# Performance work log

Hardware: AMD Instinct MI355X
Metric: run time of the kernel (lower is better)

The kernel has to match this reference:

```python
import math
import jax, jax.numpy as jnp
import numpy as np

NUM_HEADS = 16
INPUT_DIM = 1024
VALUES_DIM = 1024
HEAD_DIM = INPUT_DIM // NUM_HEADS


def _pos_embeddings(length, dim):
    # TENER positional encoding for `length` positions centered at 0: [length, dim]
    half = dim // 2
    position = jnp.arange(-(length // 2), length // 2, dtype=jnp.float32)[:, None]
    div_term = jnp.exp(jnp.arange(half, dtype=jnp.float32) * (-math.log(10000.0) / (half - 1)))
    ang = position * div_term[None, :]
    return jnp.concatenate([jnp.sin(ang), jnp.cos(ang)], axis=1)


def _shift(t):
    # [B,H,S,2S] -> [B,H,S,S] relative-position shift trick
    B, H, S, _ = t.shape
    t = jnp.concatenate([t, jnp.zeros((B, H, S, 1), t.dtype)], axis=-1)  # [B,H,S,2S+1]
    t = t.reshape(B, H, 2 * S + 1, S)[:, :, :-1].reshape(B, H, S, 2 * S)
    return t[..., S:]


def setup_inputs() -> dict:
    key = jax.random.key(0)
    ks = jax.random.split(key, 9)
    B, S, D, Dv = 2, 1024, INPUT_DIM, VALUES_DIM
    s = 1.0 / math.sqrt(D)
    return {
        "query": jax.random.normal(ks[0], (B, S, D), jnp.float32),
        "key": jax.random.normal(ks[1], (B, S, D), jnp.float32),
        "value": jax.random.normal(ks[2], (B, S, D), jnp.float32),
        "mask": jnp.ones((B, S), jnp.int32),
        "Wq": jax.random.normal(ks[3], (D, D), jnp.float32) * s,
        "bq": jnp.zeros((D,), jnp.float32),
        "Wv": jax.random.normal(ks[4], (Dv, D), jnp.float32) * s,
        "bv": jnp.zeros((Dv,), jnp.float32),
        "Wo": jax.random.normal(ks[5], (D, Dv), jnp.float32) * (1.0 / math.sqrt(Dv)),
        "bo": jnp.zeros((D,), jnp.float32),
        "v_bias": jax.random.normal(ks[6], (NUM_HEADS, HEAD_DIM), jnp.float32) * (1.0 / math.sqrt(HEAD_DIM)),
    }


def reference(query, key, value, mask, Wq, bq, Wv, bv, Wo, bo, v_bias):
    B, S, D = query.shape
    H, d = NUM_HEADS, HEAD_DIM
    dv = VALUES_DIM // H
    pos = _pos_embeddings(2 * S, d)  # [2S, d]

    k = key.reshape(B, S, H, d).transpose(0, 2, 1, 3)                       # [B,H,S,d] (no projection!)
    q = (query @ Wq.T + bq).reshape(B, S, H, d).transpose(0, 2, 1, 3)       # [B,H,S,d]
    v = (value @ Wv.T + bv).reshape(B, S, H, dv).transpose(0, 2, 1, 3)      # [B,H,S,dv]

    qk = jnp.einsum('bhqd,bhkd->bhqk', q, k)                                # [B,H,S,S]
    v_bias_rel = jnp.einsum('hd,ld->hl', v_bias, pos)[None, :, None, :]     # [1,H,1,2S]
    q_rel = jnp.einsum('bhqd,ld->bhql', q, pos)                             # [B,H,S,2S]
    rel = _shift(q_rel + v_bias_rel)                                        # [B,H,S,S]

    attn = jax.nn.softmax(qk + rel, axis=-1)                                # unscaled, unmasked (matches source)
    x = jnp.einsum('bhqk,bhkd->bhqd', attn, v)                              # [B,H,S,dv]
    x = x.transpose(0, 2, 1, 3).reshape(B, S, VALUES_DIM)
    return x @ Wo.T + bo
```

## Files before the change

### kernel.cpp

```cpp
#include <hip/hip_runtime.h>
#include <math.h>

#define SEQ 1024
#define DIM 1024
#define NH 16
#define HD 64
#define NB 2

typedef __attribute__((ext_vector_type(8))) short bf16x8;
typedef __attribute__((ext_vector_type(8))) _Float16 f16x8;
typedef __attribute__((ext_vector_type(4))) float f32x4;
typedef __attribute__((ext_vector_type(8))) unsigned short ushort8;
typedef __attribute__((ext_vector_type(4))) unsigned short ushort4v;

#define DT_CONST (-0.2971077539347156f)
#define FIXEDM 32.0f

__device__ __forceinline__ unsigned short f2bf(float x) {
    unsigned u = __float_as_uint(x);
    return (unsigned short)((u + 0x7fffu + ((u >> 16) & 1u)) >> 16);
}
__device__ __forceinline__ float bf2f(unsigned short h) {
    return __uint_as_float(((unsigned)h) << 16);
}
__device__ __forceinline__ unsigned short f2h(float x) {
    _Float16 h = (_Float16)x;
    return __builtin_bit_cast(unsigned short, h);
}

__device__ __forceinline__ void plain8(const float* __restrict__ s,
                                       unsigned short* __restrict__ h, int i) {
    float4 v0 = *(const float4*)&s[i];
    float4 v1 = *(const float4*)&s[i + 4];
    float vs[8] = {v0.x, v0.y, v0.z, v0.w, v1.x, v1.y, v1.z, v1.w};
    ushort8 hv;
    #pragma unroll
    for (int k = 0; k < 8; ++k) hv[k] = f2bf(vs[k]);
    *(ushort8*)&h[i] = hv;
}
__device__ __forceinline__ void plain8h(const float* __restrict__ s,
                                        unsigned short* __restrict__ h, int i) {
    float4 v0 = *(const float4*)&s[i];
    float4 v1 = *(const float4*)&s[i + 4];
    float vs[8] = {v0.x, v0.y, v0.z, v0.w, v1.x, v1.y, v1.z, v1.w};
    ushort8 hv;
    #pragma unroll
    for (int k = 0; k < 8; ++k) hv[k] = f2h(vs[k]);
    *(ushort8*)&h[i] = hv;
}

__global__ __launch_bounds__(256) void conv_all(
    const float* __restrict__ query, const float* __restrict__ key,
    const float* __restrict__ value, const float* __restrict__ Wq,
    const float* __restrict__ Wv, const float* __restrict__ Wo,
    unsigned short* __restrict__ Aqh,
    unsigned short* __restrict__ Khs,
    unsigned short* __restrict__ Vb,
    unsigned short* __restrict__ Wqh,
    unsigned short* __restrict__ Wvh,
    unsigned short* __restrict__ Woh,
    unsigned short* __restrict__ Kth)
{
    int i = (blockIdx.x * 256 + threadIdx.x) * 8;
    int r = blockIdx.y;
    const int NSMALL = DIM * DIM;
    if (r >= 3 && r <= 5 && i >= NSMALL) return;
    if (r == 6 && i >= SEQ * HD) return;
    switch (r) {
        case 0: plain8h(query, Aqh, i); break;
        case 1: plain8h(key,   Khs, i); break;
        case 2: plain8(value, Vb, i); break;
        case 3: plain8h(Wq, Wqh, i); break;
        case 4: plain8(Wv, Wvh, i); break;
        case 5: plain8(Wo, Woh, i); break;
        case 6: {
            ushort8 hv;
            #pragma unroll
            for (int k = 0; k < 8; ++k) {
                int idx = i + k;
                int j = idx >> 6;
                int c = idx & 63;
                int ii = c & 31;
                float dt = __expf((float)ii * DT_CONST);
                float ang = (float)j * dt;
                float val = (c < 32) ? sinf(ang) : cosf(ang);
                hv[k] = f2h(val);
            }
            *(ushort8*)&Kth[i] = hv;
            break;
        }
    }
}

#define QLD 72

__global__ __launch_bounds__(256) void qv_gemm(
    const unsigned short* __restrict__ Aqh, const unsigned short* __restrict__ Wqh,
    const float* __restrict__ bq,
    const unsigned short* __restrict__ Vb, const unsigned short* __restrict__ Wvh,
    const float* __restrict__ bv,
    const float* __restrict__ v_bias,
    unsigned short* __restrict__ Qh,
    unsigned short* __restrict__ vpT)
{
    __shared__ __align__(16) unsigned short smem[192 * QLD];
    unsigned short* sAh = smem;
    unsigned short* sWh = smem + 128 * QLD;

    const int K = DIM;
    bool isq = (blockIdx.z == 0);

    int tid = threadIdx.x;
    int lane = tid & 63;
    int w = tid >> 6;
    int l16 = lane & 15, quad = lane >> 4;
    int m0 = blockIdx.y * 128;
    int h = blockIdx.x;
    int n0 = h * 64;

    int ar = tid >> 2;
    int c0 = (tid & 3) << 3;
    int c1 = c0 + 32;

    const unsigned short* pAh0 = (isq ? Aqh : Vb) + (size_t)(m0 + ar) * K;
    const unsigned short* pAh1 = pAh0 + (size_t)64 * K;
    const unsigned short* pWh  = (isq ? Wqh : Wvh) + (size_t)(n0 + ar) * K;

    f32x4 acc[2][4];
    #pragma unroll
    for (int mq = 0; mq < 2; ++mq)
        #pragma unroll
        for (int nt = 0; nt < 4; ++nt)
            acc[mq][nt] = (f32x4){0.f, 0.f, 0.f, 0.f};

    ushort8 ra[4], rw[2];
    ra[0] = *(const ushort8*)(pAh0 + c0);  ra[1] = *(const ushort8*)(pAh0 + c1);
    ra[2] = *(const ushort8*)(pAh1 + c0);  ra[3] = *(const ushort8*)(pAh1 + c1);
    rw[0] = *(const ushort8*)(pWh + c0);   rw[1] = *(const ushort8*)(pWh + c1);

    for (int kk = 0; kk < K; kk += 64) {
        __syncthreads();
        *(ushort8*)&sAh[ar * QLD + c0] = ra[0];
        *(ushort8*)&sAh[ar * QLD + c1] = ra[1];
        *(ushort8*)&sAh[(ar + 64) * QLD + c0] = ra[2];
        *(ushort8*)&sAh[(ar + 64) * QLD + c1] = ra[3];
        *(ushort8*)&sWh[ar * QLD + c0] = rw[0];
        *(ushort8*)&sWh[ar * QLD + c1] = rw[1];
        if (kk + 64 < K) {
            int kn = kk + 64;
            ra[0] = *(const ushort8*)(pAh0 + kn + c0);  ra[1] = *(const ushort8*)(pAh0 + kn + c1);
            ra[2] = *(const ushort8*)(pAh1 + kn + c0);  ra[3] = *(const ushort8*)(pAh1 + kn + c1);
            rw[0] = *(const ushort8*)(pWh + kn + c0);   rw[1] = *(const ushort8*)(pWh + kn + c1);
        }
        __syncthreads();

        #pragma unroll
        for (int c = 0; c < 2; ++c) {
            int kpos = c * 32 + quad * 8;
            bf16x8 af[2];
            #pragma unroll
            for (int mq = 0; mq < 2; ++mq)
                af[mq] = *(const bf16x8*)&sAh[(w * 32 + mq * 16 + l16) * QLD + kpos];
            bf16x8 bhv[4];
            #pragma unroll
            for (int nt = 0; nt < 4; ++nt)
                bhv[nt] = *(const bf16x8*)&sWh[(nt * 16 + l16) * QLD + kpos];
            if (isq) {
                #pragma unroll
                for (int nt = 0; nt < 4; ++nt)
                    #pragma unroll
                    for (int mq = 0; mq < 2; ++mq)
                        acc[mq][nt] = __builtin_amdgcn_mfma_f32_16x16x32_f16(
                            __builtin_bit_cast(f16x8, af[mq]),
                            __builtin_bit_cast(f16x8, bhv[nt]), acc[mq][nt], 0, 0, 0);
            } else {
                #pragma unroll
                for (int nt = 0; nt < 4; ++nt)
                    #pragma unroll
                    for (int mq = 0; mq < 2; ++mq)
                        acc[mq][nt] = __builtin_amdgcn_mfma_f32_16x16x32_bf16(
                            af[mq], bhv[nt], acc[mq][nt], 0, 0, 0);
            }
        }
    }

    int b = m0 >> 10;

    if (isq) {
        float bql[4], vbs[2], vbc[2], dti[2];
        #pragma unroll
        for (int nt = 0; nt < 4; ++nt) bql[nt] = bq[h * 64 + nt * 16 + l16];
        #pragma unroll
        for (int t = 0; t < 2; ++t) {
            vbs[t] = v_bias[h * 64 + t * 16 + l16];
            vbc[t] = v_bias[h * 64 + 32 + t * 16 + l16];
            dti[t] = __expf((float)(t * 16 + l16) * DT_CONST);
        }
        #pragma unroll
        for (int mq = 0; mq < 2; ++mq) {
            #pragma unroll
            for (int reg = 0; reg < 4; ++reg) {
                int row = m0 + w * 32 + mq * 16 + quad * 4 + reg;
                int q = row & (SEQ - 1);
                size_t qbase = ((size_t)(b * NH + h) * SEQ + q) * 128;
                float hv[4];
                #pragma unroll
                for (int nt = 0; nt < 4; ++nt) hv[nt] = acc[mq][nt][reg] + bql[nt];
                #pragma unroll
                for (int nt = 0; nt < 4; ++nt)
                    Qh[qbase + nt * 16 + l16] = f2h(hv[nt]);
                #pragma unroll
                for (int t = 0; t < 2; ++t) {
                    float u = hv[t] + vbs[t];
                    float wv = hv[t + 2] + vbc[t];
                    float ang = (float)q * dti[t];
                    float C = cosf(ang), S = sinf(ang);
                    float cs = u * C + wv * S;
                    float cc = wv * C - u * S;
                    Qh[qbase + 64 + t * 16 + l16] = f2h(cs);
                    Qh[qbase + 96 + t * 16 + l16] = f2h(cc);
                }
            }
        }
    } else {
        __syncthreads();
        unsigned short* tb = smem;
        #pragma unroll
        for (int nt = 0; nt < 4; ++nt) {
            int d = nt * 16 + l16;
            float bcol = bv[n0 + d];
            #pragma unroll
            for (int mq = 0; mq < 2; ++mq)
                #pragma unroll
                for (int reg = 0; reg < 4; ++reg) {
                    int srow = w * 32 + mq * 16 + quad * 4 + reg;
                    tb[d * 136 + srow] = f2bf(acc[mq][nt][reg] + bcol);
                }
        }
        __syncthreads();
        int s0 = m0 & (SEQ - 1);
        #pragma unroll
        for (int i = tid; i < 1024; i += 256) {
            int dd = i >> 4;
            int j16 = i & 15;
            int sb = j16 >> 3;
            int posl = (j16 & 7) << 3;
            unsigned short tmp[8];
            #pragma unroll
            for (int k = 0; k < 8; ++k) {
                int pos = posl + k;
                int sl = (pos >> 2) + (pos & 3) * 16;
                tmp[k] = tb[dd * 136 + sb * 64 + sl];
            }
            *(ushort8*)&vpT[((size_t)((b * NH + h) * 64 + dd)) * SEQ + s0 + sb * 64 + posl] =
                *(ushort8*)tmp;
        }
    }
}

__global__ __launch_bounds__(256) void out_gemm(
    const unsigned short* __restrict__ Ab, const unsigned short* __restrict__ Woh,
    const float* __restrict__ bo, float* __restrict__ C)
{
    __shared__ unsigned short sA[64][32];
    __shared__ unsigned short sW[64][32];

    const int K = DIM, N = DIM;
    int tid = threadIdx.x;
    int lane = tid & 63;
    int w = tid >> 6;
    int l16 = lane & 15, quad = lane >> 4;
    int m0 = blockIdx.y * 64, n0 = blockIdx.x * 64;

    int ar = tid >> 2, ap = (tid & 3) << 3;

    const unsigned short* pA = Ab + (size_t)(m0 + ar) * K + ap;
    const unsigned short* pW = Woh + (size_t)(n0 + ar) * K + ap;

    f32x4 acc[4];
    #pragma unroll
    for (int nt = 0; nt < 4; ++nt) acc[nt] = (f32x4){0.f, 0.f, 0.f, 0.f};

    ushort8 a0 = *(const ushort8*)pA;
    ushort8 w0 = *(const ushort8*)pW;

    for (int kk = 0; kk < K; kk += 32) {
        __syncthreads();
        *(ushort8*)&sA[ar][ap] = a0;
        *(ushort8*)&sW[ar][ap] = w0;
        if (kk + 32 < K) {
            a0 = *(const ushort8*)(pA + kk + 32);
            w0 = *(const ushort8*)(pW + kk + 32);
        }
        __syncthreads();

        bf16x8 af = *(const bf16x8*)&sA[w * 16 + l16][quad * 8];
        bf16x8 bf[4];
        #pragma unroll
        for (int nt = 0; nt < 4; ++nt)
            bf[nt] = *(const bf16x8*)&sW[nt * 16 + l16][quad * 8];
        #pragma unroll
        for (int nt = 0; nt < 4; ++nt)
            acc[nt] = __builtin_amdgcn_mfma_f32_16x16x32_bf16(af, bf[nt], acc[nt], 0, 0, 0);
    }

    #pragma unroll
    for (int nt = 0; nt < 4; ++nt) {
        int col = n0 + nt * 16 + l16;
        float bcol = bo[col];
        #pragma unroll
        for (int reg = 0; reg < 4; ++reg) {
            int row = m0 + w * 16 + quad * 4 + reg;
            C[(size_t)row * N + col] = acc[nt][reg] + bcol;
        }
    }
}

#define LDK 136
#define LDV 72

__global__ __launch_bounds__(256) void attn_mfma(
    const unsigned short* __restrict__ Kh,
    const unsigned short* __restrict__ vpT,
    const unsigned short* __restrict__ Qh,
    const unsigned short* __restrict__ Kth,
    unsigned short* __restrict__ Opart,
    float* __restrict__ lsum)
{
    __shared__ unsigned short Ksh[64][LDK];
    __shared__ unsigned short Vt[64][LDV];
    __shared__ unsigned short Ps[128][LDV];

    int tid = threadIdx.x;
    int w = tid >> 6;
    int lane = tid & 63;
    int l16 = lane & 15;
    int quad = lane >> 4;

    int bid = blockIdx.x;
    int qt = bid & 7;
    int h = (bid >> 3) & 15;
    int b = (bid >> 7) & 1;
    int sp = bid >> 8;
    int q0 = qt << 7;
    int jb = sp << 3;

    int sr0 = tid >> 3, sp0 = (tid & 7) << 3;
    int sr1 = sr0 + 32;

    ushort8 pK0, pK1, pT0, pT1, pV0, pV1;
    {
        int j0 = jb << 6;
        size_t g0 = (size_t)(b * SEQ + j0 + sr0) * DIM + h * HD + sp0;
        size_t g1 = (size_t)(b * SEQ + j0 + sr1) * DIM + h * HD + sp0;
        pK0 = *(const ushort8*)&Kh[g0]; pK1 = *(const ushort8*)&Kh[g1];
        size_t t0 = (size_t)(j0 + sr0) * 64 + sp0, t1 = (size_t)(j0 + sr1) * 64 + sp0;
        pT0 = *(const ushort8*)&Kth[t0]; pT1 = *(const ushort8*)&Kth[t1];
        size_t v0 = ((size_t)((b * NH + h) * 64 + sr0)) * SEQ + j0 + sp0;
        size_t v1 = ((size_t)((b * NH + h) * 64 + sr1)) * SEQ + j0 + sp0;
        pV0 = *(const ushort8*)&vpT[v0]; pV1 = *(const ushort8*)&vpT[v1];
    }

    bf16x8 ah[2][4];
    #pragma unroll
    for (int half = 0; half < 2; ++half) {
        const unsigned short* gq = Qh + (((size_t)(b * NH + h)) * SEQ + q0 + half * 64) * 128;
        #pragma unroll
        for (int c = tid; c < 1024; c += 256) {
            int r = c >> 4, p = (c & 15) << 3;
            *(ushort8*)&Ksh[r][p] = *(const ushort8*)&gq[r * 128 + p];
        }
        __syncthreads();
        if ((w >> 1) == half) {
            #pragma unroll
            for (int mq = 0; mq < 2; ++mq)
                #pragma unroll
                for (int c = 0; c < 4; ++c)
                    ah[mq][c] = *(const bf16x8*)&Ksh[(w & 1) * 32 + mq * 16 + l16][c * 32 + quad * 8];
        }
        __syncthreads();
    }

    f32x4 oacc[2][4];
    f32x4 lacc[2];
    #pragma unroll
    for (int mq = 0; mq < 2; ++mq) {
        #pragma unroll
        for (int nb = 0; nb < 4; ++nb) oacc[mq][nb] = (f32x4){0.f, 0.f, 0.f, 0.f};
        lacc[mq] = (f32x4){0.f, 0.f, 0.f, 0.f};
    }

    bf16x8 onesv;
    #pragma unroll
    for (int k = 0; k < 8; ++k) onesv[k] = (short)0x3F80;

    for (int jt = 0; jt < 8; ++jt) {
        __syncthreads();
        *(ushort8*)&Ksh[sr0][sp0] = pK0;       *(ushort8*)&Ksh[sr1][sp0] = pK1;
        *(ushort8*)&Ksh[sr0][64 + sp0] = pT0;  *(ushort8*)&Ksh[sr1][64 + sp0] = pT1;
        *(ushort8*)&Vt[sr0][sp0] = pV0;        *(ushort8*)&Vt[sr1][sp0] = pV1;
        if (jt < 7) {
            int j0n = (jb + jt + 1) << 6;
            size_t g0 = (size_t)(b * SEQ + j0n + sr0) * DIM + h * HD + sp0;
            size_t g1 = (size_t)(b * SEQ + j0n + sr1) * DIM + h * HD + sp0;
            pK0 = *(const ushort8*)&Kh[g0]; pK1 = *(const ushort8*)&Kh[g1];
            size_t t0 = (size_t)(j0n + sr0) * 64 + sp0, t1 = (size_t)(j0n + sr1) * 64 + sp0;
            pT0 = *(const ushort8*)&Kth[t0]; pT1 = *(const ushort8*)&Kth[t1];
            size_t v0 = ((size_t)((b * NH + h) * 64 + sr0)) * SEQ + j0n + sp0;
            size_t v1 = ((size_t)((b * NH + h) * 64 + sr1)) * SEQ + j0n + sp0;
            pV0 = *(const ushort8*)&vpT[v0]; pV1 = *(const ushort8*)&vpT[v1];
        }
        __syncthreads();

        f32x4 sacc[2][4];
        #pragma unroll
        for (int mq = 0; mq < 2; ++mq)
            #pragma unroll
            for (int nb = 0; nb < 4; ++nb) sacc[mq][nb] = (f32x4){0.f, 0.f, 0.f, 0.f};
        #pragma unroll
        for (int nb = 0; nb < 4; ++nb) {
            #pragma unroll
            for (int c = 0; c < 4; ++c) {
                bf16x8 bh = *(const bf16x8*)&Ksh[nb * 16 + l16][c * 32 + quad * 8];
                #pragma unroll
                for (int mq = 0; mq < 2; ++mq)
                    sacc[mq][nb] = __builtin_amdgcn_mfma_f32_16x16x32_f16(
                        __builtin_bit_cast(f16x8, ah[mq][c]),
                        __builtin_bit_cast(f16x8, bh), sacc[mq][nb], 0, 0, 0);
            }
        }

        #pragma unroll
        for (int mq = 0; mq < 2; ++mq) {
            #pragma unroll
            for (int r = 0; r < 4; ++r) {
                float p0 = __expf(sacc[mq][0][r] - FIXEDM);
                float p1 = __expf(sacc[mq][1][r] - FIXEDM);
                float p2 = __expf(sacc[mq][2][r] - FIXEDM);
                float p3 = __expf(sacc[mq][3][r] - FIXEDM);
                int prow = w * 32 + mq * 16 + quad * 4 + r;
                ushort4v pv4;
                pv4.x = f2bf(p0); pv4.y = f2bf(p1); pv4.z = f2bf(p2); pv4.w = f2bf(p3);
                *(ushort4v*)&Ps[prow][l16 * 4] = pv4;
            }
        }
        __syncthreads();

        #pragma unroll
        for (int kc = 0; kc < 2; ++kc) {
            bf16x8 a[2];
            #pragma unroll
            for (int mq = 0; mq < 2; ++mq) {
                a[mq] = *(const bf16x8*)&Ps[w * 32 + mq * 16 + l16][kc * 32 + quad * 8];
                lacc[mq] = __builtin_amdgcn_mfma_f32_16x16x32_bf16(a[mq], onesv, lacc[mq], 0, 0, 0);
            }
            #pragma unroll
            for (int nb = 0; nb < 4; ++nb) {
                bf16x8 bv = *(const bf16x8*)&Vt[nb * 16 + l16][kc * 32 + quad * 8];
                #pragma unroll
                for (int mq = 0; mq < 2; ++mq)
                    oacc[mq][nb] = __builtin_amdgcn_mfma_f32_16x16x32_bf16(a[mq], bv, oacc[mq][nb], 0, 0, 0);
            }
        }
    }

    const size_t OOFF = (size_t)sp * NB * NH * SEQ * 64;
    const size_t LOFF = (size_t)sp * NB * NH * SEQ;
    #pragma unroll
    for (int mq = 0; mq < 2; ++mq) {
        #pragma unroll
        for (int r = 0; r < 4; ++r) {
            int qrow = q0 + w * 32 + mq * 16 + quad * 4 + r;
            size_t rowi = (size_t)(b * NH + h) * SEQ + qrow;
            #pragma unroll
            for (int nb = 0; nb < 4; ++nb)
                Opart[OOFF + rowi * 64 + nb * 16 + l16] = f2bf(oacc[mq][nb][r]);
            if (l16 == 0)
                lsum[LOFF + rowi] = lacc[mq][r];
        }
    }
}

__global__ __launch_bounds__(256) void attn_combine(
    const unsigned short* __restrict__ Opart, const float* __restrict__ lsum,
    unsigned short* __restrict__ xab)
{
    const size_t OOFF = (size_t)NB * NH * SEQ * 64;
    const size_t LOFF = (size_t)NB * NH * SEQ;
    int tid = threadIdx.x;
    int d = tid & 63;
    size_t r = (size_t)blockIdx.x * 4 + (tid >> 6);
    int q = (int)(r & (SEQ - 1));
    int h = (int)((r >> 10) & (NH - 1));
    int b = (int)(r >> 14);

    float inv = 1.f / (lsum[r] + lsum[LOFF + r]);
    float O0 = bf2f(Opart[r * 64 + d]);
    float O1 = bf2f(Opart[OOFF + r * 64 + d]);
    float o = (O0 + O1) * inv;
    xab[((size_t)(b * SEQ + q)) * DIM + h * HD + d] = f2bf(o);
}

extern "C" void kernel_launch(void* const* d_in, const int* in_sizes, int n_in,
                              void* d_out, int out_size, void* d_ws, size_t ws_size,
                              hipStream_t stream) {
    const float* query  = (const float*)d_in[0];
    const float* key    = (const float*)d_in[1];
    const float* value  = (const float*)d_in[2];
    const float* Wq     = (const float*)d_in[4];
    const float* bq     = (const float*)d_in[5];
    const float* Wv     = (const float*)d_in[6];
    const float* bv     = (const float*)d_in[7];
    const float* Wo     = (const float*)d_in[8];
    const float* bo     = (const float*)d_in[9];
    const float* v_bias = (const float*)d_in[10];

    float* out = (float*)d_out;
    char* base = (char*)d_ws;
    const size_t MB = 1024 * 1024;

    unsigned short* Aqh   = (unsigned short*)(base);
    unsigned short* vpT   = (unsigned short*)(base +  4 * MB);
    unsigned short* Khs   = (unsigned short*)(base +  8 * MB);
    unsigned short* Qh    = (unsigned short*)(base + 12 * MB);
    unsigned short* Wqh   = (unsigned short*)(base + 20 * MB);
    unsigned short* Vb    = (unsigned short*)(base + 22 * MB);
    unsigned short* Wvh   = (unsigned short*)(base + 26 * MB);
    unsigned short* Woh   = (unsigned short*)(base + 28 * MB);
    unsigned short* Kth   = (unsigned short*)(base + 30 * MB);
    unsigned short* xab   = (unsigned short*)(base + 31 * MB);
    float*          lsum  = (float*)(base + 35 * MB);
    unsigned short* Opart = (unsigned short*)(base + 36 * MB);

    const int M = NB * SEQ;

    dim3 cgrid(M * DIM / 2048, 7);
    conv_all<<<cgrid, 256, 0, stream>>>(query, key, value, Wq, Wv, Wo,
                                        Aqh, Khs, Vb, Wqh, Wvh, Woh, Kth);

    dim3 qvgrid(NH, M / 128, 2);
    qv_gemm<<<qvgrid, 256, 0, stream>>>(Aqh, Wqh, bq, Vb, Wvh, bv,
                                        v_bias, Qh, vpT);

    attn_mfma<<<2 * NB * NH * (SEQ / 128), 256, 0, stream>>>(Khs, vpT, Qh,
                                                             Kth, Opart, lsum);

    attn_combine<<<NB * NH * SEQ / 4, 256, 0, stream>>>(Opart, lsum, xab);

    dim3 ogrid(DIM / 64, M / 64);
    out_gemm<<<ogrid, 256, 0, stream>>>(xab, Woh, bo, out);
}
```

Measured before the change: 158.3 us.

## Remap block indices for L2 locality and widen out_gemm K-step to 64

Converts the qv_gemm, attn_mfma and out_gemm grids to 1D launches and remaps block IDs. The new order groups blocks that share input tiles, and on a multi-XCD GPU places related work on the same die for better L2 reuse. out_gemm now stages 64-wide K tiles with padded shared-memory rows, which halves the number of barrier pairs and avoids bank conflicts. This costs more shared memory and registers per block and depends on assumptions about how blocks are dispatched across dies.

```diff
diff --git a/kernel.cpp b/kernel.cpp
--- a/kernel.cpp
+++ b/kernel.cpp
@@ -108,15 +108,19 @@
     unsigned short* sWh = smem + 128 * QLD;
 
     const int K = DIM;
-    bool isq = (blockIdx.z == 0);
+
+    int bid = blockIdx.x;
+    int s = bid >> 3;
+    int y = (bid & 7) + 8 * (s & 1);
+    int h = (s >> 1) & 15;
+    bool isq = (s >> 5) == 0;
+    int m0 = y * 128;
+    int n0 = h * 64;
 
     int tid = threadIdx.x;
     int lane = tid & 63;
     int w = tid >> 6;
     int l16 = lane & 15, quad = lane >> 4;
-    int m0 = blockIdx.y * 128;
-    int h = blockIdx.x;
-    int n0 = h * 64;
 
     int ar = tid >> 2;
     int c0 = (tid & 3) << 3;
@@ -262,46 +266,58 @@
     const unsigned short* __restrict__ Ab, const unsigned short* __restrict__ Woh,
     const float* __restrict__ bo, float* __restrict__ C)
 {
-    __shared__ unsigned short sA[64][32];
-    __shared__ unsigned short sW[64][32];
+    __shared__ __align__(16) unsigned short sA[64 * QLD];
+    __shared__ __align__(16) unsigned short sW[64 * QLD];
 
     const int K = DIM, N = DIM;
+
+    int bid = blockIdx.x;
+    int n0 = ((bid >> 3) & 15) * 64;
+    int m0 = ((bid & 7) + 8 * (bid >> 7)) * 64;
+
     int tid = threadIdx.x;
     int lane = tid & 63;
     int w = tid >> 6;
     int l16 = lane & 15, quad = lane >> 4;
-    int m0 = blockIdx.y * 64, n0 = blockIdx.x * 64;
-
-    int ar = tid >> 2, ap = (tid & 3) << 3;
-
-    const unsigned short* pA = Ab + (size_t)(m0 + ar) * K + ap;
-    const unsigned short* pW = Woh + (size_t)(n0 + ar) * K + ap;
+
+    int ar = tid >> 2;
+    int c0 = (tid & 3) << 3;
+    int c1 = c0 + 32;
+
+    const unsigned short* pA = Ab + (size_t)(m0 + ar) * K;
+    const unsigned short* pW = Woh + (size_t)(n0 + ar) * K;
 
     f32x4 acc[4];
     #pragma unroll
     for (int nt = 0; nt < 4; ++nt) acc[nt] = (f32x4){0.f, 0.f, 0.f, 0.f};
 
-    ushort8 a0 = *(const ushort8*)pA;
-    ushort8 w0 = *(const ushort8*)pW;
-
-    for (int kk = 0; kk < K; kk += 32) {
-        __syncthreads();
-        *(ushort8*)&sA[ar][ap] = a0;
-        *(ushort8*)&sW[ar][ap] = w0;
-        if (kk + 32 < K) {
-            a0 = *(const ushort8*)(pA + kk + 32);
-            w0 = *(const ushort8*)(pW + kk + 32);
-        }
-        __syncthreads();
-
-        bf16x8 af = *(const bf16x8*)&sA[w * 16 + l16][quad * 8];
-        bf16x8 bf[4];
-        #pragma unroll
-        for (int nt = 0; nt < 4; ++nt)
-            bf[nt] = *(const bf16x8*)&sW[nt * 16 + l16][quad * 8];
-        #pragma unroll
-        for (int nt = 0; nt < 4; ++nt)
-            acc[nt] = __builtin_amdgcn_mfma_f32_16x16x32_bf16(af, bf[nt], acc[nt], 0, 0, 0);
+    ushort8 ra[2], rw[2];
+    ra[0] = *(const ushort8*)(pA + c0);  ra[1] = *(const ushort8*)(pA + c1);
+    rw[0] = *(const ushort8*)(pW + c0);  rw[1] = *(const ushort8*)(pW + c1);
+
+    for (int kk = 0; kk < K; kk += 64) {
+        __syncthreads();
+        *(ushort8*)&sA[ar * QLD + c0] = ra[0];
+        *(ushort8*)&sA[ar * QLD + c1] = ra[1];
+        *(ushort8*)&sW[ar * QLD + c0] = rw[0];
+        *(ushort8*)&sW[ar * QLD + c1] = rw[1];
+        if (kk + 64 < K) {
+            int kn = kk + 64;
+            ra[0] = *(const ushort8*)(pA + kn + c0);  ra[1] = *(const ushort8*)(pA + kn + c1);
+            rw[0] = *(const ushort8*)(pW + kn + c0);  rw[1] = *(const ushort8*)(pW + kn + c1);
+        }
+        __syncthreads();
+
+        #pragma unroll
+        for (int c = 0; c < 2; ++c) {
+            int kpos = c * 32 + quad * 8;
+            bf16x8 af = *(const bf16x8*)&sA[(w * 16 + l16) * QLD + kpos];
+            #pragma unroll
+            for (int nt = 0; nt < 4; ++nt) {
+                bf16x8 bh = *(const bf16x8*)&sW[(nt * 16 + l16) * QLD + kpos];
+                acc[nt] = __builtin_amdgcn_mfma_f32_16x16x32_bf16(af, bh, acc[nt], 0, 0, 0);
+            }
+        }
     }
 
     #pragma unroll
@@ -338,10 +354,11 @@
     int quad = lane >> 4;
 
     int bid = blockIdx.x;
-    int qt = bid & 7;
-    int h = (bid >> 3) & 15;
-    int b = (bid >> 7) & 1;
-    int sp = bid >> 8;
+    int g = bid & 63;
+    int qt = bid >> 6;
+    int h = g & 15;
+    int b = (g >> 4) & 1;
+    int sp = g >> 5;
     int q0 = qt << 7;
     int jb = sp << 3;
 
@@ -538,15 +555,12 @@
     conv_all<<<cgrid, 256, 0, stream>>>(query, key, value, Wq, Wv, Wo,
                                         Aqh, Khs, Vb, Wqh, Wvh, Woh, Kth);
 
-    dim3 qvgrid(NH, M / 128, 2);
-    qv_gemm<<<qvgrid, 256, 0, stream>>>(Aqh, Wqh, bq, Vb, Wvh, bv,
-                                        v_bias, Qh, vpT);
-
-    attn_mfma<<<2 * NB * NH * (SEQ / 128), 256, 0, stream>>>(Khs, vpT, Qh,
-                                                             Kth, Opart, lsum);
+    qv_gemm<<<512, 256, 0, stream>>>(Aqh, Wqh, bq, Vb, Wvh, bv,
+                                     v_bias, Qh, vpT);
+
+    attn_mfma<<<512, 256, 0, stream>>>(Khs, vpT, Qh, Kth, Opart, lsum);
 
     attn_combine<<<NB * NH * SEQ / 4, 256, 0, stream>>>(Opart, lsum, xab);
 
-    dim3 ogrid(DIM / 64, M / 64);
-    out_gemm<<<ogrid, 256, 0, stream>>>(xab, Woh, bo, out);
-}
+    out_gemm<<<512, 256, 0, stream>>>(xab, Woh, bo, out);
+}
```

Measured after the change: 157.4 us. About the same (-0.6%).

## Fuse input conversions into consumer GEMMs and fold split-combine into output GEMM

Applied to the files above, without the earlier changes.

Removes the standalone conversion pass that turned fp32 query/key/value/weights into half/bf16 copies. Each consumer kernel (qv_gemm, attn_mfma, the output GEMM) now loads fp32 directly and converts while writing to shared memory. The attention split-combine kernel is merged into the output projection, which normalizes the two partial outputs on the fly. This cuts several launches and the round-trip of intermediate buffers through memory. In exchange, global loads inside the GEMM loops are twice as wide and conversion ALU work is repeated across tiles that reread the same data.

```diff
diff --git a/kernel.cpp b/kernel.cpp
--- a/kernel.cpp
+++ b/kernel.cpp
@@ -27,77 +27,43 @@
     _Float16 h = (_Float16)x;
     return __builtin_bit_cast(unsigned short, h);
 }
-
-__device__ __forceinline__ void plain8(const float* __restrict__ s,
-                                       unsigned short* __restrict__ h, int i) {
-    float4 v0 = *(const float4*)&s[i];
-    float4 v1 = *(const float4*)&s[i + 4];
-    float vs[8] = {v0.x, v0.y, v0.z, v0.w, v1.x, v1.y, v1.z, v1.w};
-    ushort8 hv;
-    #pragma unroll
-    for (int k = 0; k < 8; ++k) hv[k] = f2bf(vs[k]);
-    *(ushort8*)&h[i] = hv;
-}
-__device__ __forceinline__ void plain8h(const float* __restrict__ s,
-                                        unsigned short* __restrict__ h, int i) {
-    float4 v0 = *(const float4*)&s[i];
-    float4 v1 = *(const float4*)&s[i + 4];
-    float vs[8] = {v0.x, v0.y, v0.z, v0.w, v1.x, v1.y, v1.z, v1.w};
-    ushort8 hv;
-    #pragma unroll
-    for (int k = 0; k < 8; ++k) hv[k] = f2h(vs[k]);
-    *(ushort8*)&h[i] = hv;
-}
-
-__global__ __launch_bounds__(256) void conv_all(
-    const float* __restrict__ query, const float* __restrict__ key,
-    const float* __restrict__ value, const float* __restrict__ Wq,
-    const float* __restrict__ Wv, const float* __restrict__ Wo,
-    unsigned short* __restrict__ Aqh,
-    unsigned short* __restrict__ Khs,
-    unsigned short* __restrict__ Vb,
-    unsigned short* __restrict__ Wqh,
-    unsigned short* __restrict__ Wvh,
-    unsigned short* __restrict__ Woh,
-    unsigned short* __restrict__ Kth)
+__device__ __forceinline__ ushort8 cvt8h(float4 a, float4 b) {
+    ushort8 r;
+    r[0] = f2h(a.x); r[1] = f2h(a.y); r[2] = f2h(a.z); r[3] = f2h(a.w);
+    r[4] = f2h(b.x); r[5] = f2h(b.y); r[6] = f2h(b.z); r[7] = f2h(b.w);
+    return r;
+}
+__device__ __forceinline__ ushort8 cvt8b(float4 a, float4 b) {
+    ushort8 r;
+    r[0] = f2bf(a.x); r[1] = f2bf(a.y); r[2] = f2bf(a.z); r[3] = f2bf(a.w);
+    r[4] = f2bf(b.x); r[5] = f2bf(b.y); r[6] = f2bf(b.z); r[7] = f2bf(b.w);
+    return r;
+}
+
+__global__ __launch_bounds__(256) void trig_gen(unsigned short* __restrict__ Kth)
 {
     int i = (blockIdx.x * 256 + threadIdx.x) * 8;
-    int r = blockIdx.y;
-    const int NSMALL = DIM * DIM;
-    if (r >= 3 && r <= 5 && i >= NSMALL) return;
-    if (r == 6 && i >= SEQ * HD) return;
-    switch (r) {
-        case 0: plain8h(query, Aqh, i); break;
-        case 1: plain8h(key,   Khs, i); break;
-        case 2: plain8(value, Vb, i); break;
-        case 3: plain8h(Wq, Wqh, i); break;
-        case 4: plain8(Wv, Wvh, i); break;
-        case 5: plain8(Wo, Woh, i); break;
-        case 6: {
-            ushort8 hv;
-            #pragma unroll
-            for (int k = 0; k < 8; ++k) {
-                int idx = i + k;
-                int j = idx >> 6;
-                int c = idx & 63;
-                int ii = c & 31;
-                float dt = __expf((float)ii * DT_CONST);
-                float ang = (float)j * dt;
-                float val = (c < 32) ? sinf(ang) : cosf(ang);
-                hv[k] = f2h(val);
-            }
-            *(ushort8*)&Kth[i] = hv;
-            break;
-        }
-    }
+    ushort8 hv;
+    #pragma unroll
+    for (int k = 0; k < 8; ++k) {
+        int idx = i + k;
+        int j = idx >> 6;
+        int c = idx & 63;
+        int ii = c & 31;
+        float dt = __expf((float)ii * DT_CONST);
+        float ang = (float)j * dt;
+        float val = (c < 32) ? sinf(ang) : cosf(ang);
+        hv[k] = f2h(val);
+    }
+    *(ushort8*)&Kth[i] = hv;
 }
 
 #define QLD 72
 
 __global__ __launch_bounds__(256) void qv_gemm(
-    const unsigned short* __restrict__ Aqh, const unsigned short* __restrict__ Wqh,
+    const float* __restrict__ query, const float* __restrict__ Wq,
     const float* __restrict__ bq,
-    const unsigned short* __restrict__ Vb, const unsigned short* __restrict__ Wvh,
+    const float* __restrict__ value, const float* __restrict__ Wv,
     const float* __restrict__ bv,
     const float* __restrict__ v_bias,
     unsigned short* __restrict__ Qh,
@@ -122,9 +88,9 @@
     int c0 = (tid & 3) << 3;
     int c1 = c0 + 32;
 
-    const unsigned short* pAh0 = (isq ? Aqh : Vb) + (size_t)(m0 + ar) * K;
-    const unsigned short* pAh1 = pAh0 + (size_t)64 * K;
-    const unsigned short* pWh  = (isq ? Wqh : Wvh) + (size_t)(n0 + ar) * K;
+    const float* pA0 = (isq ? query : value) + (size_t)(m0 + ar) * K;
+    const float* pA1 = pA0 + (size_t)64 * K;
+    const float* pW  = (isq ? Wq : Wv) + (size_t)(n0 + ar) * K;
 
     f32x4 acc[2][4];
     #pragma unroll
@@ -133,24 +99,39 @@
         for (int nt = 0; nt < 4; ++nt)
             acc[mq][nt] = (f32x4){0.f, 0.f, 0.f, 0.f};
 
-    ushort8 ra[4], rw[2];
-    ra[0] = *(const ushort8*)(pAh0 + c0);  ra[1] = *(const ushort8*)(pAh0 + c1);
-    ra[2] = *(const ushort8*)(pAh1 + c0);  ra[3] = *(const ushort8*)(pAh1 + c1);
-    rw[0] = *(const ushort8*)(pWh + c0);   rw[1] = *(const ushort8*)(pWh + c1);
+    float4 rf[6][2];
+    rf[0][0] = *(const float4*)(pA0 + c0); rf[0][1] = *(const float4*)(pA0 + c0 + 4);
+    rf[1][0] = *(const float4*)(pA0 + c1); rf[1][1] = *(const float4*)(pA0 + c1 + 4);
+    rf[2][0] = *(const float4*)(pA1 + c0); rf[2][1] = *(const float4*)(pA1 + c0 + 4);
+    rf[3][0] = *(const float4*)(pA1 + c1); rf[3][1] = *(const float4*)(pA1 + c1 + 4);
+    rf[4][0] = *(const float4*)(pW + c0);  rf[4][1] = *(const float4*)(pW + c0 + 4);
+    rf[5][0] = *(const float4*)(pW + c1);  rf[5][1] = *(const float4*)(pW + c1 + 4);
 
     for (int kk = 0; kk < K; kk += 64) {
         __syncthreads();
-        *(ushort8*)&sAh[ar * QLD + c0] = ra[0];
-        *(ushort8*)&sAh[ar * QLD + c1] = ra[1];
-        *(ushort8*)&sAh[(ar + 64) * QLD + c0] = ra[2];
-        *(ushort8*)&sAh[(ar + 64) * QLD + c1] = ra[3];
-        *(ushort8*)&sWh[ar * QLD + c0] = rw[0];
-        *(ushort8*)&sWh[ar * QLD + c1] = rw[1];
+        if (isq) {
+            *(ushort8*)&sAh[ar * QLD + c0]        = cvt8h(rf[0][0], rf[0][1]);
+            *(ushort8*)&sAh[ar * QLD + c1]        = cvt8h(rf[1][0], rf[1][1]);
+            *(ushort8*)&sAh[(ar + 64) * QLD + c0] = cvt8h(rf[2][0], rf[2][1]);
+            *(ushort8*)&sAh[(ar + 64) * QLD + c1] = cvt8h(rf[3][0], rf[3][1]);
+            *(ushort8*)&sWh[ar * QLD + c0]        = cvt8h(rf[4][0], rf[4][1]);
+            *(ushort8*)&sWh[ar * QLD + c1]        = cvt8h(rf[5][0], rf[5][1]);
+        } else {
+            *(ushort8*)&sAh[ar * QLD + c0]        = cvt8b(rf[0][0], rf[0][1]);
+            *(ushort8*)&sAh[ar * QLD + c1]        = cvt8b(rf[1][0], rf[1][1]);
+            *(ushort8*)&sAh[(ar + 64) * QLD + c0] = cvt8b(rf[2][0], rf[2][1]);
+            *(ushort8*)&sAh[(ar + 64) * QLD + c1] = cvt8b(rf[3][0], rf[3][1]);
+            *(ushort8*)&sWh[ar * QLD + c0]        = cvt8b(rf[4][0], rf[4][1]);
+            *(ushort8*)&sWh[ar * QLD + c1]        = cvt8b(rf[5][0], rf[5][1]);
+        }
         if (kk + 64 < K) {
             int kn = kk + 64;
-            ra[0] = *(const ushort8*)(pAh0 + kn + c0);  ra[1] = *(const ushort8*)(pAh0 + kn + c1);
-            ra[2] = *(const ushort8*)(pAh1 + kn + c0);  ra[3] = *(const ushort8*)(pAh1 + kn + c1);
-            rw[0] = *(const ushort8*)(pWh + kn + c0);   rw[1] = *(const ushort8*)(pWh + kn + c1);
+            rf[0][0] = *(const float4*)(pA0 + kn + c0); rf[0][1] = *(const float4*)(pA0 + kn + c0 + 4);
+            rf[1][0] = *(const float4*)(pA0 + kn + c1); rf[1][1] = *(const float4*)(pA0 + kn + c1 + 4);
+            rf[2][0] = *(const float4*)(pA1 + kn + c0); rf[2][1] = *(const float4*)(pA1 + kn + c0 + 4);
+            rf[3][0] = *(const float4*)(pA1 + kn + c1); rf[3][1] = *(const float4*)(pA1 + kn + c1 + 4);
+            rf[4][0] = *(const float4*)(pW + kn + c0);  rf[4][1] = *(const float4*)(pW + kn + c0 + 4);
+            rf[5][0] = *(const float4*)(pW + kn + c1);  rf[5][1] = *(const float4*)(pW + kn + c1 + 4);
         }
         __syncthreads();
 
@@ -258,69 +239,11 @@
     }
 }
 
-__global__ __launch_bounds__(256) void out_gemm(
-    const unsigned short* __restrict__ Ab, const unsigned short* __restrict__ Woh,
-    const float* __restrict__ bo, float* __restrict__ C)
-{
-    __shared__ unsigned short sA[64][32];
-    __shared__ unsigned short sW[64][32];
-
-    const int K = DIM, N = DIM;
-    int tid = threadIdx.x;
-    int lane = tid & 63;
-    int w = tid >> 6;
-    int l16 = lane & 15, quad = lane >> 4;
-    int m0 = blockIdx.y * 64, n0 = blockIdx.x * 64;
-
-    int ar = tid >> 2, ap = (tid & 3) << 3;
-
-    const unsigned short* pA = Ab + (size_t)(m0 + ar) * K + ap;
-    const unsigned short* pW = Woh + (size_t)(n0 + ar) * K + ap;
-
-    f32x4 acc[4];
-    #pragma unroll
-    for (int nt = 0; nt < 4; ++nt) acc[nt] = (f32x4){0.f, 0.f, 0.f, 0.f};
-
-    ushort8 a0 = *(const ushort8*)pA;
-    ushort8 w0 = *(const ushort8*)pW;
-
-    for (int kk = 0; kk < K; kk += 32) {
-        __syncthreads();
-        *(ushort8*)&sA[ar][ap] = a0;
-        *(ushort8*)&sW[ar][ap] = w0;
-        if (kk + 32 < K) {
-            a0 = *(const ushort8*)(pA + kk + 32);
-            w0 = *(const ushort8*)(pW + kk + 32);
-        }
-        __syncthreads();
-
-        bf16x8 af = *(const bf16x8*)&sA[w * 16 + l16][quad * 8];
-        bf16x8 bf[4];
-        #pragma unroll
-        for (int nt = 0; nt < 4; ++nt)
-            bf[nt] = *(const bf16x8*)&sW[nt * 16 + l16][quad * 8];
-        #pragma unroll
-        for (int nt = 0; nt < 4; ++nt)
-            acc[nt] = __builtin_amdgcn_mfma_f32_16x16x32_bf16(af, bf[nt], acc[nt], 0, 0, 0);
-    }
-
-    #pragma unroll
-    for (int nt = 0; nt < 4; ++nt) {
-        int col = n0 + nt * 16 + l16;
-        float bcol = bo[col];
-        #pragma unroll
-        for (int reg = 0; reg < 4; ++reg) {
-            int row = m0 + w * 16 + quad * 4 + reg;
-            C[(size_t)row * N + col] = acc[nt][reg] + bcol;
-        }
-    }
-}
-
 #define LDK 136
 #define LDV 72
 
 __global__ __launch_bounds__(256) void attn_mfma(
-    const unsigned short* __restrict__ Kh,
+    const float* __restrict__ key,
     const unsigned short* __restrict__ vpT,
     const unsigned short* __restrict__ Qh,
     const unsigned short* __restrict__ Kth,
@@ -348,12 +271,14 @@
     int sr0 = tid >> 3, sp0 = (tid & 7) << 3;
     int sr1 = sr0 + 32;
 
-    ushort8 pK0, pK1, pT0, pT1, pV0, pV1;
+    float4 kf0a, kf0b, kf1a, kf1b;
+    ushort8 pT0, pT1, pV0, pV1;
     {
         int j0 = jb << 6;
         size_t g0 = (size_t)(b * SEQ + j0 + sr0) * DIM + h * HD + sp0;
         size_t g1 = (size_t)(b * SEQ + j0 + sr1) * DIM + h * HD + sp0;
-        pK0 = *(const ushort8*)&Kh[g0]; pK1 = *(const ushort8*)&Kh[g1];
+        kf0a = *(const float4*)&key[g0]; kf0b = *(const float4*)&key[g0 + 4];
+        kf1a = *(const float4*)&key[g1]; kf1b = *(const float4*)&key[g1 + 4];
         size_t t0 = (size_t)(j0 + sr0) * 64 + sp0, t1 = (size_t)(j0 + sr1) * 64 + sp0;
         pT0 = *(const ushort8*)&Kth[t0]; pT1 = *(const ushort8*)&Kth[t1];
         size_t v0 = ((size_t)((b * NH + h) * 64 + sr0)) * SEQ + j0 + sp0;
@@ -396,14 +321,16 @@
 
     for (int jt = 0; jt < 8; ++jt) {
         __syncthreads();
-        *(ushort8*)&Ksh[sr0][sp0] = pK0;       *(ushort8*)&Ksh[sr1][sp0] = pK1;
+        *(ushort8*)&Ksh[sr0][sp0] = cvt8h(kf0a, kf0b);
+        *(ushort8*)&Ksh[sr1][sp0] = cvt8h(kf1a, kf1b);
         *(ushort8*)&Ksh[sr0][64 + sp0] = pT0;  *(ushort8*)&Ksh[sr1][64 + sp0] = pT1;
         *(ushort8*)&Vt[sr0][sp0] = pV0;        *(ushort8*)&Vt[sr1][sp0] = pV1;
         if (jt < 7) {
             int j0n = (jb + jt + 1) << 6;
             size_t g0 = (size_t)(b * SEQ + j0n + sr0) * DIM + h * HD + sp0;
             size_t g1 = (size_t)(b * SEQ + j0n + sr1) * DIM + h * HD + sp0;
-            pK0 = *(const ushort8*)&Kh[g0]; pK1 = *(const ushort8*)&Kh[g1];
+            kf0a = *(const float4*)&key[g0]; kf0b = *(const float4*)&key[g0 + 4];
+            kf1a = *(const float4*)&key[g1]; kf1b = *(const float4*)&key[g1 + 4];
             size_t t0 = (size_t)(j0n + sr0) * 64 + sp0, t1 = (size_t)(j0n + sr1) * 64 + sp0;
             pT0 = *(const ushort8*)&Kth[t0]; pT1 = *(const ushort8*)&Kth[t1];
             size_t v0 = ((size_t)((b * NH + h) * 64 + sr0)) * SEQ + j0n + sp0;
@@ -481,24 +408,102 @@
     }
 }
 
-__global__ __launch_bounds__(256) void attn_combine(
+__global__ __launch_bounds__(256) void out_fused(
     const unsigned short* __restrict__ Opart, const float* __restrict__ lsum,
-    unsigned short* __restrict__ xab)
+    const float* __restrict__ Wo, const float* __restrict__ bo,
+    float* __restrict__ C)
 {
+    __shared__ __align__(16) unsigned short sA[64 * QLD];
+    __shared__ __align__(16) unsigned short sW[64 * QLD];
+
+    const int K = DIM, N = DIM;
     const size_t OOFF = (size_t)NB * NH * SEQ * 64;
     const size_t LOFF = (size_t)NB * NH * SEQ;
+
+    int m0 = blockIdx.y * 64, n0 = blockIdx.x * 64;
+
     int tid = threadIdx.x;
-    int d = tid & 63;
-    size_t r = (size_t)blockIdx.x * 4 + (tid >> 6);
-    int q = (int)(r & (SEQ - 1));
-    int h = (int)((r >> 10) & (NH - 1));
-    int b = (int)(r >> 14);
-
-    float inv = 1.f / (lsum[r] + lsum[LOFF + r]);
-    float O0 = bf2f(Opart[r * 64 + d]);
-    float O1 = bf2f(Opart[OOFF + r * 64 + d]);
-    float o = (O0 + O1) * inv;
-    xab[((size_t)(b * SEQ + q)) * DIM + h * HD + d] = f2bf(o);
+    int lane = tid & 63;
+    int w = tid >> 6;
+    int l16 = lane & 15, quad = lane >> 4;
+
+    int ar = tid >> 2;
+    int c0 = (tid & 3) << 3;
+    int c1 = c0 + 32;
+
+    int grow = m0 + ar;
+    int gb = grow >> 10, gq = grow & (SEQ - 1);
+
+    const float* pW = Wo + (size_t)(n0 + ar) * K;
+
+    f32x4 acc[4];
+    #pragma unroll
+    for (int nt = 0; nt < 4; ++nt) acc[nt] = (f32x4){0.f, 0.f, 0.f, 0.f};
+
+    ushort8 o0a, o1a, o0b, o1b;
+    float l0, l1;
+    float4 wf[2][2];
+    {
+        size_t rowi = (size_t)(gb * NH + 0) * SEQ + gq;
+        o0a = *(const ushort8*)&Opart[rowi * 64 + c0];
+        o1a = *(const ushort8*)&Opart[OOFF + rowi * 64 + c0];
+        o0b = *(const ushort8*)&Opart[rowi * 64 + c1];
+        o1b = *(const ushort8*)&Opart[OOFF + rowi * 64 + c1];
+        l0 = lsum[rowi]; l1 = lsum[LOFF + rowi];
+        wf[0][0] = *(const float4*)(pW + c0); wf[0][1] = *(const float4*)(pW + c0 + 4);
+        wf[1][0] = *(const float4*)(pW + c1); wf[1][1] = *(const float4*)(pW + c1 + 4);
+    }
+
+    for (int kk = 0; kk < K; kk += 64) {
+        __syncthreads();
+        float inv = 1.f / (l0 + l1);
+        ushort8 av;
+        #pragma unroll
+        for (int k = 0; k < 8; ++k)
+            av[k] = f2bf((bf2f(o0a[k]) + bf2f(o1a[k])) * inv);
+        *(ushort8*)&sA[ar * QLD + c0] = av;
+        #pragma unroll
+        for (int k = 0; k < 8; ++k)
+            av[k] = f2bf((bf2f(o0b[k]) + bf2f(o1b[k])) * inv);
+        *(ushort8*)&sA[ar * QLD + c1] = av;
+        *(ushort8*)&sW[ar * QLD + c0] = cvt8b(wf[0][0], wf[0][1]);
+        *(ushort8*)&sW[ar * QLD + c1] = cvt8b(wf[1][0], wf[1][1]);
+        if (kk + 64 < K) {
+            int kn = kk + 64;
+            int h = kn >> 6;
+            size_t rowi = (size_t)(gb * NH + h) * SEQ + gq;
+            o0a = *(const ushort8*)&Opart[rowi * 64 + c0];
+            o1a = *(const ushort8*)&Opart[OOFF + rowi * 64 + c0];
+            o0b = *(const ushort8*)&Opart[rowi * 64 + c1];
+            o1b = *(const ushort8*)&Opart[OOFF + rowi * 64 + c1];
+            l0 = lsum[rowi]; l1 = lsum[LOFF + rowi];
+            wf[0][0] = *(const float4*)(pW + kn + c0); wf[0][1] = *(const float4*)(pW + kn + c0 + 4);
+            wf[1][0] = *(const float4*)(pW + kn + c1); wf[1][1] = *(const float4*)(pW + kn + c1 + 4);
+        }
+        __syncthreads();
+
+        #pragma unroll
+        for (int c = 0; c < 2; ++c) {
+            int kpos = c * 32 + quad * 8;
+            bf16x8 af = *(const bf16x8*)&sA[(w * 16 + l16) * QLD + kpos];
+            #pragma unroll
+            for (int nt = 0; nt < 4; ++nt) {
+                bf16x8 bh = *(const bf16x8*)&sW[(nt * 16 + l16) * QLD + kpos];
+                acc[nt] = __builtin_amdgcn_mfma_f32_16x16x32_bf16(af, bh, acc[nt], 0, 0, 0);
+            }
+        }
+    }
+
+    #pragma unroll
+    for (int nt = 0; nt < 4; ++nt) {
+        int col = n0 + nt * 16 + l16;
+        float bcol = bo[col];
+        #pragma unroll
+        for (int reg = 0; reg < 4; ++reg) {
+            int row = m0 + w * 16 + quad * 4 + reg;
+            C[(size_t)row * N + col] = acc[nt][reg] + bcol;
+        }
+    }
 }
 
 extern "C" void kernel_launch(void* const* d_in, const int* in_sizes, int n_in,
@@ -519,34 +524,23 @@
     char* base = (char*)d_ws;
     const size_t MB = 1024 * 1024;
 
-    unsigned short* Aqh   = (unsigned short*)(base);
-    unsigned short* vpT   = (unsigned short*)(base +  4 * MB);
-    unsigned short* Khs   = (unsigned short*)(base +  8 * MB);
-    unsigned short* Qh    = (unsigned short*)(base + 12 * MB);
-    unsigned short* Wqh   = (unsigned short*)(base + 20 * MB);
-    unsigned short* Vb    = (unsigned short*)(base + 22 * MB);
-    unsigned short* Wvh   = (unsigned short*)(base + 26 * MB);
-    unsigned short* Woh   = (unsigned short*)(base + 28 * MB);
-    unsigned short* Kth   = (unsigned short*)(base + 30 * MB);
-    unsigned short* xab   = (unsigned short*)(base + 31 * MB);
-    float*          lsum  = (float*)(base + 35 * MB);
-    unsigned short* Opart = (unsigned short*)(base + 36 * MB);
+    unsigned short* vpT   = (unsigned short*)(base);
+    unsigned short* Qh    = (unsigned short*)(base +  4 * MB);
+    unsigned short* Kth   = (unsigned short*)(base + 12 * MB);
+    float*          lsum  = (float*)(base + 13 * MB);
+    unsigned short* Opart = (unsigned short*)(base + 14 * MB);
 
     const int M = NB * SEQ;
 
-    dim3 cgrid(M * DIM / 2048, 7);
-    conv_all<<<cgrid, 256, 0, stream>>>(query, key, value, Wq, Wv, Wo,
-                                        Aqh, Khs, Vb, Wqh, Wvh, Woh, Kth);
+    trig_gen<<<SEQ * HD / 2048, 256, 0, stream>>>(Kth);
 
     dim3 qvgrid(NH, M / 128, 2);
-    qv_gemm<<<qvgrid, 256, 0, stream>>>(Aqh, Wqh, bq, Vb, Wvh, bv,
+    qv_gemm<<<qvgrid, 256, 0, stream>>>(query, Wq, bq, value, Wv, bv,
                                         v_bias, Qh, vpT);
 
-    attn_mfma<<<2 * NB * NH * (SEQ / 128), 256, 0, stream>>>(Khs, vpT, Qh,
+    attn_mfma<<<2 * NB * NH * (SEQ / 128), 256, 0, stream>>>(key, vpT, Qh,
                                                              Kth, Opart, lsum);
 
-    attn_combine<<<NB * NH * SEQ / 4, 256, 0, stream>>>(Opart, lsum, xab);
-
     dim3 ogrid(DIM / 64, M / 64);
-    out_gemm<<<ogrid, 256, 0, stream>>>(xab, Woh, bo, out);
-}
+    out_fused<<<ogrid, 256, 0, stream>>>(Opart, lsum, Wo, bo, out);
+}
```

Result: slower. 167.1 us (+5.6%).
